# Performance work log

Measured on AMD Instinct MI355X. Metric: run time of the kernel, lower is better.

The kernel has to match this reference:

```python
import jax, jax.numpy as jnp
import numpy as np

B, N, C, H = 4, 1024, 1024, 16
DH = C // H  # 64
EPS = 1e-5   # nn.LayerNorm default


def _layernorm(x, g, b):
    m = x.mean(-1, keepdims=True)
    v = ((x - m) ** 2).mean(-1, keepdims=True)
    return (x - m) * jax.lax.rsqrt(v + EPS) * g + b


def _rot_half(x):
    d = x.shape[-1] // 2
    return jnp.concatenate([-x[..., d:], x[..., :d]], axis=-1)


def _apply_rope_cat(x, emb):
    # emb: [N, 2*DH] = sin || cos (torch tensor_split(2, -1) order)
    sin, cos = jnp.split(emb, 2, axis=-1)  # each [N, DH]
    return x * cos + _rot_half(x) * sin


def setup_inputs() -> dict:
    key = jax.random.key(0)
    ks = jax.random.split(key, 12)
    s = 0.02
    x = jax.random.normal(ks[0], (B, N, C), jnp.float32)
    delta_t_emb = jax.random.normal(ks[1], (B, N, C), jnp.float32)
    v_residual_v1 = jax.random.normal(ks[2], (B, H, N, DH), jnp.float32)
    # realistic rope table: sin||cos, each DH wide (freqs repeated twice for rotate_half)
    pos = jnp.arange(N, dtype=jnp.float32)
    inv_freq = 1.0 / (10000.0 ** (jnp.arange(0, DH // 2, dtype=jnp.float32) / (DH // 2)))
    freqs = pos[:, None] * inv_freq[None, :]          # [N, DH/2]
    freqs = jnp.concatenate([freqs, freqs], axis=-1)  # [N, DH]
    rope = jnp.concatenate([jnp.sin(freqs), jnp.cos(freqs)], axis=-1)  # [N, 2*DH]
    Wqkv = jax.random.normal(ks[3], (3 * C, C), jnp.float32) * s
    bqkv = jnp.zeros((3 * C,), jnp.float32)
    Wdt = jax.random.normal(ks[4], (3 * C, C), jnp.float32) * s
    bdt = jnp.zeros((3 * C,), jnp.float32)
    qn_g = jnp.ones((DH,), jnp.float32); qn_b = jnp.zeros((DH,), jnp.float32)
    kn_g = jnp.ones((DH,), jnp.float32); kn_b = jnp.zeros((DH,), jnp.float32)
    lamb1 = jnp.asarray(0.5, jnp.float32)
    lamb2 = jnp.asarray(0.5, jnp.float32)
    Wproj = jax.random.normal(ks[5], (C, C), jnp.float32) * s
    bproj = jnp.zeros((C,), jnp.float32)
    return {
        "x": x, "rope": rope, "delta_t_emb": delta_t_emb, "v_residual_v1": v_residual_v1,
        "Wqkv": Wqkv, "bqkv": bqkv, "Wdt": Wdt, "bdt": bdt,
        "qn_g": qn_g, "qn_b": qn_b, "kn_g": kn_g, "kn_b": kn_b,
        "lamb1": lamb1, "lamb2": lamb2, "Wproj": Wproj, "bproj": bproj,
    }


def reference(x, rope, delta_t_emb, v_residual_v1, Wqkv, bqkv, Wdt, bdt,
              qn_g, qn_b, kn_g, kn_b, lamb1, lamb2, Wproj, bproj):
    b, n, c = x.shape
    # fused QKV: [B,N,3C] -> [3,B,H,N,DH]
    qkv = (jnp.einsum('bnc,oc->bno', x, Wqkv) + bqkv).reshape(b, n, 3, H, DH)
    qkv = jnp.transpose(qkv, (2, 0, 3, 1, 4))
    q, k, v = qkv[0], qkv[1], qkv[2]
    # delta-t additive embeddings
    dqkv = (jnp.einsum('bnc,oc->bno', delta_t_emb, Wdt) + bdt).reshape(b, n, 3, H, DH)
    dqkv = jnp.transpose(dqkv, (2, 0, 3, 1, 4))
    q = q + dqkv[0]; k = k + dqkv[1]; v = v + dqkv[2]
    # value-residual mixing
    v = lamb1 * v + lamb2 * v_residual_v1
    # qk layernorm over head_dim
    q = _layernorm(q, qn_g, qn_b)
    k = _layernorm(k, kn_g, kn_b)
    # RoPE (num_prefix_tokens = 0, rotate_half=True)
    q = _apply_rope_cat(q, rope)
    k = _apply_rope_cat(k, rope)
    # SDPA, non-causal, no dropout
    scale = 1.0 / jnp.sqrt(jnp.asarray(DH, x.dtype))
    scores = jnp.einsum('bhqd,bhkd->bhqk', q, k) * scale
    attn = jax.nn.softmax(scores, axis=-1)
    out = jnp.einsum('bhqk,bhkd->bhqd', attn, v)
    # [B,H,N,DH] -> [B,N,C], output norm is Identity (scale_norm=False)
    out = jnp.transpose(out, (0, 2, 1, 3)).reshape(b, n, c)
    out = jnp.einsum('bnc,oc->bno', out, Wproj) + bproj
    return out
```

## Files before the change

### kernel.cpp

```cpp
#include <hip/hip_runtime.h>
#include <stdint.h>

typedef unsigned short u16;
typedef __attribute__((ext_vector_type(8))) short short8;
typedef __attribute__((ext_vector_type(4))) float f32x4;
typedef __attribute__((ext_vector_type(4))) unsigned short u16x4;

#define DEVI __device__ __forceinline__

DEVI u16 f2bf(float f) {
  uint32_t u = __builtin_bit_cast(uint32_t, f);
  u += 0x7fffu + ((u >> 16) & 1u);
  return (u16)(u >> 16);
}

DEVI void gload_lds16(const void* g, void* l) {
  __builtin_amdgcn_global_load_lds(
      (const __attribute__((address_space(1))) void*)g,
      (__attribute__((address_space(3))) void*)(uint32_t)(uintptr_t)l,
      16, 0, 0);
}

__global__ void cvt_cat_bf16(const float* __restrict__ a, const float* __restrict__ b,
                             u16* __restrict__ dst, long total) {
  for (long i = ((long)blockIdx.x * 256 + threadIdx.x) * 4; i < total;
       i += (long)gridDim.x * 1024) {
    const long row = i >> 11;
    const long c = i & 2047;
    const float* src = (c < 1024) ? (a + row * 1024 + c) : (b + row * 1024 + (c - 1024));
    const float4 v = *(const float4*)src;
    u16x4 o = {f2bf(v.x), f2bf(v.y), f2bf(v.z), f2bf(v.w)};
    *(u16x4*)(dst + i) = o;
  }
}

__global__ void cvt_bf16(const float* __restrict__ a, u16* __restrict__ dst, long total) {
  for (long i = ((long)blockIdx.x * 256 + threadIdx.x) * 4; i < total;
       i += (long)gridDim.x * 1024) {
    const float4 v = *(const float4*)(a + i);
    u16x4 o = {f2bf(v.x), f2bf(v.y), f2bf(v.z), f2bf(v.w)};
    *(u16x4*)(dst + i) = o;
  }
}

__global__ __launch_bounds__(256, 2)
void gemm_bt(const u16* __restrict__ A, const u16* __restrict__ B,
             float* __restrict__ C, const float* __restrict__ bias1,
             const float* __restrict__ bias2, int M, int N, int K) {
  __shared__ u16 As[128 * 32];
  __shared__ u16 Bs[128 * 32];
  const int t = threadIdx.x;
  const int w = t >> 6, l = t & 63;
  const int l15 = l & 15, lg = l >> 4;
  const int bm = blockIdx.x, bn = blockIdx.y;
  const int wr = (w >> 1) * 64, wc = (w & 1) * 64;
  f32x4 acc[4][4] = {};
  const int c0 = w * 64 + l;

  for (int kt = 0; kt < (K >> 5); ++kt) {
#pragma unroll
    for (int i = 0; i < 2; ++i) {
      const int c = i * 256 + c0;
      const int row = c >> 2, seg = c & 3;
      gload_lds16(A + (long)(bm * 128 + row) * K + kt * 32 + seg * 8,
                  (char*)As + w * 1024 + i * 4096);
      gload_lds16(B + (long)(bn * 128 + row) * K + kt * 32 + seg * 8,
                  (char*)Bs + w * 1024 + i * 4096);
    }
    __syncthreads();
    short8 af[4], bfr[4];
#pragma unroll
    for (int m = 0; m < 4; ++m)
      af[m] = *(const short8*)&As[(wr + m * 16 + l15) * 32 + lg * 8];
#pragma unroll
    for (int n = 0; n < 4; ++n)
      bfr[n] = *(const short8*)&Bs[(wc + n * 16 + l15) * 32 + lg * 8];
#pragma unroll
    for (int m = 0; m < 4; ++m)
#pragma unroll
      for (int n = 0; n < 4; ++n)
        acc[m][n] = __builtin_amdgcn_mfma_f32_16x16x32_bf16(af[m], bfr[n], acc[m][n], 0, 0, 0);
    __syncthreads();
  }
#pragma unroll
  for (int m = 0; m < 4; ++m) {
    const int row0 = bm * 128 + wr + m * 16 + lg * 4;
#pragma unroll
    for (int n = 0; n < 4; ++n) {
      const int col = bn * 128 + wc + n * 16 + l15;
      float bia = 0.f;
      if (bias1) bia += bias1[col];
      if (bias2) bia += bias2[col];
#pragma unroll
      for (int r = 0; r < 4; ++r)
        C[(long)(row0 + r) * N + col] = acc[m][n][r] + bia;
    }
  }
}

__global__ __launch_bounds__(256)
void fuse_qkv2(const float* __restrict__ qkv, const float* __restrict__ vres,
               const float* __restrict__ rope,
               const float* __restrict__ qg, const float* __restrict__ qb,
               const float* __restrict__ kg, const float* __restrict__ kb,
               const float* __restrict__ pl1, const float* __restrict__ pl2,
               u16* __restrict__ Q, u16* __restrict__ Ksw, u16* __restrict__ VTsw) {
  __shared__ u16 Vl[64][72];
  const int t = threadIdx.x, w = t >> 6, d = t & 63;
  const int bh = blockIdx.x, ntile = blockIdx.y;
  const int b = bh >> 4, h = bh & 15, n0 = ntile * 64;
  const float l1 = pl1[0], l2 = pl2[0];
  const float gq = qg[d], bq = qb[d];
  const float gk = kg[d], bk = kb[d];
  const float sgn = (d < 32) ? -1.f : 1.f;
  const int c = d >> 3, d7 = d & 7;

  for (int i = 0; i < 16; ++i) {
    const int nl = w * 16 + i;
    const int n = n0 + nl;
    const long base = ((long)(b * 1024 + n)) * 3072 + h * 64 + d;
    float q = qkv[base];
    float k = qkv[base + 1024];
    float v = qkv[base + 2048];
    v = l1 * v + l2 * vres[((long)(bh * 1024 + n)) * 64 + d];
    const float sinv = rope[n * 128 + d];
    const float cosv = rope[n * 128 + 64 + d];
    float s = q;
#pragma unroll
    for (int off = 1; off < 64; off <<= 1) s += __shfl_xor(s, off);
    const float qc = q - s * (1.f / 64.f);
    float vs = qc * qc;
#pragma unroll
    for (int off = 1; off < 64; off <<= 1) vs += __shfl_xor(vs, off);
    const float qn = qc * (1.f / sqrtf(vs * (1.f / 64.f) + 1e-5f)) * gq + bq;
    float s2 = k;
#pragma unroll
    for (int off = 1; off < 64; off <<= 1) s2 += __shfl_xor(s2, off);
    const float kc = k - s2 * (1.f / 64.f);
    float vs2 = kc * kc;
#pragma unroll
    for (int off = 1; off < 64; off <<= 1) vs2 += __shfl_xor(vs2, off);
    const float kn = kc * (1.f / sqrtf(vs2 * (1.f / 64.f) + 1e-5f)) * gk + bk;
    const float qo = __shfl_xor(qn, 32);
    const float ko = __shfl_xor(kn, 32);
    const float qr = qn * cosv + sgn * qo * sinv;
    const float kr = kn * cosv + sgn * ko * sinv;
    Q[(long)bh * 65536 + (long)n * 64 + d] = f2bf(qr);
    Ksw[(long)bh * 65536 + (long)n * 64 + ((c ^ (n & 7)) * 8 + d7)] = f2bf(kr);
    Vl[nl][d] = f2bf(v);
  }
  __syncthreads();
#pragma unroll
  for (int i = 0; i < 2; ++i) {
    const int task = i * 256 + t;
    const int dd = task >> 3, cc = task & 7;
    short8 o;
#pragma unroll
    for (int u = 0; u < 8; ++u) o[u] = (short)Vl[cc * 8 + u][dd];
    *(short8*)&VTsw[((long)(bh * 64 + dd)) * 1024 + n0 + ((cc ^ (dd & 7)) * 8)] = o;
  }
}

__global__ __launch_bounds__(256, 4)
void attn_fwd2(const u16* __restrict__ Q, const u16* __restrict__ Ksw,
               const u16* __restrict__ VTsw, u16* __restrict__ Out) {
  __shared__ u16 Kl[64 * 64];
  __shared__ u16 Vl[64 * 64];
  __shared__ u16 Pl[4][16 * 64];
  const int t = threadIdx.x, w = t >> 6, l = t & 63;
  const int l15 = l & 15, lg = l >> 4;
  const int x7 = l15 & 7;
  const int bh = blockIdx.x, q0 = blockIdx.y * 64;
  const long bo = (long)bh * 65536;
  u16* Plw = &Pl[w][0];

  const int qrow = q0 + w * 16 + l15;
  short8 qf[2];
#pragma unroll
  for (int ks = 0; ks < 2; ++ks)
    qf[ks] = *(const short8*)&Q[bo + (long)qrow * 64 + ks * 32 + lg * 8];

  f32x4 acc[4] = {};
  float m_run = -1e30f, l_run = 0.f;

  for (int kv = 0; kv < 16; ++kv) {
    const int kvb = kv * 64;
#pragma unroll
    for (int i = 0; i < 2; ++i) {
      const int idx = i * 256 + t;
      const int row = idx >> 3, seg = idx & 7;
      gload_lds16(Ksw + bo + (long)(kvb + row) * 64 + seg * 8, (char*)Kl + idx * 16);
      gload_lds16(VTsw + bo + (long)row * 1024 + kvb + seg * 8, (char*)Vl + idx * 16);
    }
    __syncthreads();
    f32x4 p[4];
#pragma unroll
    for (int mt = 0; mt < 4; ++mt) {
      f32x4 ps = {};
#pragma unroll
      for (int ks = 0; ks < 2; ++ks) {
        const short8 kf =
            *(const short8*)&Kl[(mt * 16 + l15) * 64 + (((ks * 4 + lg) ^ x7) * 8)];
        ps = __builtin_amdgcn_mfma_f32_16x16x32_bf16(kf, qf[ks], ps, 0, 0, 0);
      }
      p[mt] = ps;
    }
    float mx = p[0][0];
#pragma unroll
    for (int mt = 0; mt < 4; ++mt)
#pragma unroll
      for (int r = 0; r < 4; ++r) mx = fmaxf(mx, p[mt][r]);
    mx = fmaxf(mx, __shfl_xor(mx, 16));
    mx = fmaxf(mx, __shfl_xor(mx, 32));
    const float mnew = fmaxf(m_run, mx * 0.125f);
    const float alpha = __expf(m_run - mnew);
    m_run = mnew;
    float sum = 0.f;
#pragma unroll
    for (int mt = 0; mt < 4; ++mt)
#pragma unroll
      for (int r = 0; r < 4; ++r) {
        const float e = __expf(p[mt][r] * 0.125f - mnew);
        p[mt][r] = e;
        sum += e;
      }
    sum += __shfl_xor(sum, 16);
    sum += __shfl_xor(sum, 32);
    l_run = l_run * alpha + sum;
#pragma unroll
    for (int mt = 0; mt < 4; ++mt) {
      const int c = mt * 2 + (lg >> 1);
      char* bp = (char*)Plw + l15 * 128 + ((c ^ x7) * 16) + (lg & 1) * 8;
      *(uint32_t*)bp = (uint32_t)f2bf(p[mt][0]) | ((uint32_t)f2bf(p[mt][1]) << 16);
      *(uint32_t*)(bp + 4) = (uint32_t)f2bf(p[mt][2]) | ((uint32_t)f2bf(p[mt][3]) << 16);
    }
#pragma unroll
    for (int mt = 0; mt < 4; ++mt)
#pragma unroll
      for (int r = 0; r < 4; ++r) acc[mt][r] *= alpha;
#pragma unroll
    for (int ks = 0; ks < 2; ++ks) {
      const short8 pf =
          *(const short8*)((char*)Plw + l15 * 128 + (((ks * 4 + lg) ^ x7) * 16));
#pragma unroll
      for (int mt = 0; mt < 4; ++mt) {
        const short8 vf =
            *(const short8*)&Vl[(mt * 16 + l15) * 64 + (((ks * 4 + lg) ^ x7) * 8)];
        acc[mt] = __builtin_amdgcn_mfma_f32_16x16x32_bf16(vf, pf, acc[mt], 0, 0, 0);
      }
    }
    __syncthreads();
  }
  const int b = bh >> 4, h = bh & 15;
  const float inv = 1.f / l_run;
  const long obase = ((long)(b * 1024 + qrow)) * 1024 + h * 64;
#pragma unroll
  for (int mt = 0; mt < 4; ++mt) {
    const long o = obase + mt * 16 + lg * 4;
    *(uint32_t*)&Out[o] =
        (uint32_t)f2bf(acc[mt][0] * inv) | ((uint32_t)f2bf(acc[mt][1] * inv) << 16);
    *(uint32_t*)&Out[o + 2] =
        (uint32_t)f2bf(acc[mt][2] * inv) | ((uint32_t)f2bf(acc[mt][3] * inv) << 16);
  }
}

extern "C" void kernel_launch(void* const* d_in, const int* in_sizes, int n_in,
                              void* d_out, int out_size, void* d_ws, size_t ws_size,
                              hipStream_t stream) {
  const float* x     = (const float*)d_in[0];
  const float* rope  = (const float*)d_in[1];
  const float* dte   = (const float*)d_in[2];
  const float* vres  = (const float*)d_in[3];
  const float* Wqkv  = (const float*)d_in[4];
  const float* bqkv  = (const float*)d_in[5];
  const float* Wdt   = (const float*)d_in[6];
  const float* bdt   = (const float*)d_in[7];
  const float* qn_g  = (const float*)d_in[8];
  const float* qn_b  = (const float*)d_in[9];
  const float* kn_g  = (const float*)d_in[10];
  const float* kn_b  = (const float*)d_in[11];
  const float* l1    = (const float*)d_in[12];
  const float* l2    = (const float*)d_in[13];
  const float* Wproj = (const float*)d_in[14];
  const float* bproj = (const float*)d_in[15];
  float* out = (float*)d_out;

  char* ws = (char*)d_ws;
  u16*   A_cat = (u16*)(ws);
  u16*   W_cat = (u16*)(ws + 16777216);
  u16*   Wp    = (u16*)(ws + 29360128);
  float* qkv   = (float*)(ws + 31457280);
  u16*   Qb    = (u16*)(ws + 81788928);
  u16*   Ksw   = (u16*)(ws + 90177536);
  u16*   VTsw  = (u16*)(ws + 98566144);
  u16*   AO    = (u16*)(ws + 106954752);

  cvt_cat_bf16<<<2048, 256, 0, stream>>>(x, dte, A_cat, (long)4096 * 2048);
  cvt_cat_bf16<<<2048, 256, 0, stream>>>(Wqkv, Wdt, W_cat, (long)3072 * 2048);
  cvt_bf16<<<1024, 256, 0, stream>>>(Wproj, Wp, (long)1024 * 1024);
  gemm_bt<<<dim3(32, 24), 256, 0, stream>>>(A_cat, W_cat, qkv, bqkv, bdt, 4096, 3072, 2048);
  fuse_qkv2<<<dim3(64, 16), 256, 0, stream>>>(qkv, vres, rope, qn_g, qn_b, kn_g, kn_b,
                                              l1, l2, Qb, Ksw, VTsw);
  attn_fwd2<<<dim3(64, 16), 256, 0, stream>>>(Qb, Ksw, VTsw, AO);
  gemm_bt<<<dim3(32, 8), 256, 0, stream>>>(AO, Wp, out, bproj, nullptr, 4096, 1024, 1024);
}
```

Baseline: 173.2 us.

## Add 256x256-tile pipelined GEMM with swizzled LDS for fused QKV projection

Adds a new gemm256 kernel that computes 256x256 output tiles with 512 threads and a 4-deep LDS ring buffer filled by direct global-to-LDS loads issued three K-tiles ahead, with explicit vmcnt waits. It also XOR-swizzles the LDS layout to avoid bank conflicts and remaps block IDs to group tiles for L2 locality. The QKV GEMM launch now uses this kernel instead of the 128x128 gemm_bt. The aim is more reuse per loaded byte and overlap of memory with MFMA work. In exchange it uses 128KB of LDS per block and only 192 blocks, so occupancy is low and the grid may not fill all CUs evenly.

```diff
diff --git a/kernel.cpp b/kernel.cpp
--- a/kernel.cpp
+++ b/kernel.cpp
@@ -88,6 +88,92 @@
 #pragma unroll
     for (int n = 0; n < 4; ++n) {
       const int col = bn * 128 + wc + n * 16 + l15;
+      float bia = 0.f;
+      if (bias1) bia += bias1[col];
+      if (bias2) bia += bias2[col];
+#pragma unroll
+      for (int r = 0; r < 4; ++r)
+        C[(long)(row0 + r) * N + col] = acc[m][n][r] + bia;
+    }
+  }
+}
+
+__global__ __launch_bounds__(512, 2)
+void gemm256(const u16* __restrict__ A, const u16* __restrict__ B,
+             float* __restrict__ C, const float* __restrict__ bias1,
+             const float* __restrict__ bias2, int M, int N, int K) {
+  __shared__ u16 lds[4][16384];
+  const int t = threadIdx.x;
+  const int w = t >> 6, l = t & 63;
+  const int l15 = l & 15, lg = l >> 4;
+  const int wr = w >> 2, wc = w & 3;
+  const int nbn = N >> 8;
+  const int nb = gridDim.x;
+  const int bid = blockIdx.x;
+  const int lid = ((nb & 7) == 0) ? ((bid & 7) * (nb >> 3) + (bid >> 3)) : bid;
+  const int bm = lid / nbn, bn = lid % nbn;
+  const long rowA0 = (long)bm * 256;
+  const long rowB0 = (long)bn * 256;
+  const int nkt = K >> 5;
+
+  const int su = (l & 7) ^ (l >> 3);
+  const int rsub = 2 * (l >> 3) + (su >> 2);
+  const int sg = su & 3;
+  const int sfr = (lg + 4 * (l15 & 1)) ^ (l15 >> 1);
+
+  f32x4 acc[8][4] = {};
+
+#define STAGE(KT)                                                              \
+  {                                                                            \
+    const int _b = (KT) & 3;                                                   \
+    _Pragma("unroll") for (int i = 0; i < 2; ++i) {                            \
+      const int r = i * 128 + w * 16 + rsub;                                   \
+      gload_lds16(A + (rowA0 + r) * K + (KT) * 32 + sg * 8,                    \
+                  (char*)&lds[_b][(i * 64 + w * 8) * 64]);                     \
+      gload_lds16(B + (rowB0 + r) * K + (KT) * 32 + sg * 8,                    \
+                  (char*)&lds[_b][8192 + (i * 64 + w * 8) * 64]);              \
+    }                                                                          \
+  }
+
+#define TILE(KT, VMSTR, DO_STAGE)                                              \
+  {                                                                            \
+    asm volatile("s_waitcnt vmcnt(" VMSTR ")" ::: "memory");                   \
+    __builtin_amdgcn_s_barrier();                                              \
+    asm volatile("" ::: "memory");                                             \
+    __builtin_amdgcn_sched_barrier(0);                                         \
+    if (DO_STAGE) STAGE((KT) + 3);                                             \
+    const u16* bufp = lds[(KT) & 3];                                           \
+    short8 bfr[4];                                                             \
+    _Pragma("unroll") for (int n = 0; n < 4; ++n) {                            \
+      const int p = wc * 32 + n * 8 + (l15 >> 1);                              \
+      bfr[n] = *(const short8*)&bufp[8192 + p * 64 + sfr * 8];                 \
+    }                                                                          \
+    __builtin_amdgcn_s_setprio(1);                                             \
+    _Pragma("unroll") for (int m = 0; m < 8; ++m) {                            \
+      const int p = wr * 64 + m * 8 + (l15 >> 1);                              \
+      const short8 af = *(const short8*)&bufp[p * 64 + sfr * 8];               \
+      _Pragma("unroll") for (int n = 0; n < 4; ++n)                            \
+        acc[m][n] = __builtin_amdgcn_mfma_f32_16x16x32_bf16(af, bfr[n],        \
+                                                            acc[m][n], 0, 0, 0); \
+    }                                                                          \
+    __builtin_amdgcn_s_setprio(0);                                             \
+  }
+
+  STAGE(0)
+  STAGE(1)
+  STAGE(2)
+  for (int kt = 0; kt < nkt - 2; ++kt) TILE(kt, "8", (kt + 3 < nkt))
+  TILE(nkt - 2, "4", false)
+  TILE(nkt - 1, "0", false)
+#undef TILE
+#undef STAGE
+
+#pragma unroll
+  for (int m = 0; m < 8; ++m) {
+    const int row0 = bm * 256 + wr * 128 + m * 16 + lg * 4;
+#pragma unroll
+    for (int n = 0; n < 4; ++n) {
+      const int col = bn * 256 + wc * 64 + n * 16 + l15;
       float bia = 0.f;
       if (bias1) bia += bias1[col];
       if (bias2) bia += bias2[col];
@@ -298,7 +384,7 @@
   cvt_cat_bf16<<<2048, 256, 0, stream>>>(x, dte, A_cat, (long)4096 * 2048);
   cvt_cat_bf16<<<2048, 256, 0, stream>>>(Wqkv, Wdt, W_cat, (long)3072 * 2048);
   cvt_bf16<<<1024, 256, 0, stream>>>(Wproj, Wp, (long)1024 * 1024);
-  gemm_bt<<<dim3(32, 24), 256, 0, stream>>>(A_cat, W_cat, qkv, bqkv, bdt, 4096, 3072, 2048);
+  gemm256<<<192, 512, 0, stream>>>(A_cat, W_cat, qkv, bqkv, bdt, 4096, 3072, 2048);
   fuse_qkv2<<<dim3(64, 16), 256, 0, stream>>>(qkv, vres, rope, qn_g, qn_b, kn_g, kn_b,
                                               l1, l2, Qb, Ksw, VTsw);
   attn_fwd2<<<dim3(64, 16), 256, 0, stream>>>(Qb, Ksw, VTsw, AO);
```

Result: no change. 173.6 us (+0.3%).

## Replace QKV GEMM with 256x256 pipelined kernel writing bf16 output

Applied to the files above, without the earlier changes.

Adds a new 512-thread GEMM that uses 256x256 tiles, a 4-stage LDS ring with swizzled global-to-LDS loads, split MFMA phases and XCD-aware block remapping. It is used for the fused QKV+delta-t projection, and its output is stored as bf16 instead of fp32, which halves the intermediate traffic read by fuse_qkv2. The aim is higher MFMA utilisation and less memory traffic. The cost is extra rounding of the pre-layernorm q/k/v values and only 192 blocks for the large tile size.

```diff
diff --git a/kernel.cpp b/kernel.cpp
--- a/kernel.cpp
+++ b/kernel.cpp
@@ -12,6 +12,11 @@
   uint32_t u = __builtin_bit_cast(uint32_t, f);
   u += 0x7fffu + ((u >> 16) & 1u);
   return (u16)(u >> 16);
+}
+
+DEVI float bf2f(u16 u) {
+  uint32_t v = ((uint32_t)u) << 16;
+  return __builtin_bit_cast(float, v);
 }
 
 DEVI void gload_lds16(const void* g, void* l) {
@@ -98,8 +103,147 @@
   }
 }
 
+__global__ __launch_bounds__(512, 2)
+void gemm256(const u16* __restrict__ A, const u16* __restrict__ B,
+             u16* __restrict__ Cb, const float* __restrict__ bias1,
+             const float* __restrict__ bias2, int M, int N, int K) {
+  __shared__ u16 lds[4][16384];
+  const int t = threadIdx.x;
+  const int w = t >> 6, l = t & 63;
+  const int l15 = l & 15, lg = l >> 4;
+  const int wr = w >> 2, wc = w & 3;
+  const int nbn = N >> 8;
+  const int nb = gridDim.x;
+  const int bid = blockIdx.x;
+  const int lid = ((nb & 7) == 0) ? ((bid & 7) * (nb >> 3) + (bid >> 3)) : bid;
+  const int bm = lid / nbn, bn = lid % nbn;
+  const long rowA0 = (long)bm * 256;
+  const long rowB0 = (long)bn * 256;
+  const int nkt = K >> 5;
+
+  const int su = (l & 7) ^ (l >> 3);
+  const int rsub = 2 * (l >> 3) + (su >> 2);
+  const int sg = su & 3;
+  const int sfr = (lg + 4 * (l15 & 1)) ^ (l15 >> 1);
+
+  f32x4 acc[8][4] = {};
+  short8 alo[4], ahi[4], b0[4], b1[4];
+
+#define STAGE_A(KT)                                                           \
+  {                                                                           \
+    const int _b = (KT) & 3;                                                  \
+    _Pragma("unroll") for (int i = 0; i < 2; ++i) {                           \
+      const int r = i * 128 + w * 16 + rsub;                                  \
+      gload_lds16(A + (rowA0 + r) * K + (KT) * 32 + sg * 8,                   \
+                  (char*)&lds[_b][(i * 64 + w * 8) * 64]);                    \
+    }                                                                         \
+  }
+#define STAGE_B(KT)                                                           \
+  {                                                                           \
+    const int _b = (KT) & 3;                                                  \
+    _Pragma("unroll") for (int i = 0; i < 2; ++i) {                           \
+      const int r = i * 128 + w * 16 + rsub;                                  \
+      gload_lds16(B + (rowB0 + r) * K + (KT) * 32 + sg * 8,                   \
+                  (char*)&lds[_b][8192 + (i * 64 + w * 8) * 64]);             \
+    }                                                                         \
+  }
+
+#define TILE(KT, BC, BN_, VM, LG1, DO_STAGE, DO_NEXT)                         \
+  {                                                                           \
+    const u16* bufp = lds[(KT) & 3];                                          \
+           \
+    _Pragma("unroll") for (int m = 0; m < 4; ++m) {                           \
+      const int p = wr * 64 + (m + 4) * 8 + (l15 >> 1);                       \
+      ahi[m] = *(const short8*)&bufp[p * 64 + sfr * 8];                       \
+    }                                                                         \
+    if (DO_STAGE) STAGE_A((KT) + 3);                                          \
+    asm volatile("s_waitcnt vmcnt(" VM ")" ::: "memory");                     \
+    __builtin_amdgcn_sched_barrier(0);                                        \
+    __builtin_amdgcn_s_barrier();                                             \
+    asm volatile("s_waitcnt lgkmcnt(4)" ::: "memory");                        \
+    __builtin_amdgcn_sched_barrier(0);                                        \
+    __builtin_amdgcn_s_setprio(1);                                            \
+    _Pragma("unroll") for (int m = 0; m < 4; ++m)                             \
+      _Pragma("unroll") for (int n = 0; n < 4; ++n)                           \
+        acc[m][n] = __builtin_amdgcn_mfma_f32_16x16x32_bf16(alo[m], BC[n],    \
+                                                            acc[m][n], 0, 0, 0); \
+    __builtin_amdgcn_s_setprio(0);                                            \
+    __builtin_amdgcn_sched_barrier(0);                                        \
+    __builtin_amdgcn_s_barrier();                                             \
+                    \
+    if (DO_NEXT) {                                                            \
+      const u16* bnp = lds[((KT) + 1) & 3];                                   \
+      _Pragma("unroll") for (int m = 0; m < 4; ++m) {                         \
+        const int p = wr * 64 + m * 8 + (l15 >> 1);                           \
+        alo[m] = *(const short8*)&bnp[p * 64 + sfr * 8];                      \
+      }                                                                       \
+      _Pragma("unroll") for (int n = 0; n < 4; ++n) {                         \
+        const int p = wc * 32 + n * 8 + (l15 >> 1);                           \
+        BN_[n] = *(const short8*)&bnp[8192 + p * 64 + sfr * 8];               \
+      }                                                                       \
+    }                                                                         \
+    if (DO_STAGE) STAGE_B((KT) + 3);                                          \
+    __builtin_amdgcn_sched_barrier(0);                                        \
+    __builtin_amdgcn_s_barrier();                                             \
+    asm volatile("s_waitcnt lgkmcnt(" LG1 ")" ::: "memory");                  \
+    __builtin_amdgcn_sched_barrier(0);                                        \
+    __builtin_amdgcn_s_setprio(1);                                            \
+    _Pragma("unroll") for (int m = 0; m < 4; ++m)                             \
+      _Pragma("unroll") for (int n = 0; n < 4; ++n)                           \
+        acc[m + 4][n] = __builtin_amdgcn_mfma_f32_16x16x32_bf16(              \
+            ahi[m], BC[n], acc[m + 4][n], 0, 0, 0);                           \
+    __builtin_amdgcn_s_setprio(0);                                            \
+    __builtin_amdgcn_sched_barrier(0);                                        \
+    __builtin_amdgcn_s_barrier();                                             \
+  }
+
+  STAGE_A(0); STAGE_B(0);
+  STAGE_A(1); STAGE_B(1);
+  STAGE_A(2); STAGE_B(2);
+  asm volatile("s_waitcnt vmcnt(8)" ::: "memory");
+  __builtin_amdgcn_sched_barrier(0);
+  __builtin_amdgcn_s_barrier();
+#pragma unroll
+  for (int m = 0; m < 4; ++m) {
+    const int p = wr * 64 + m * 8 + (l15 >> 1);
+    alo[m] = *(const short8*)&lds[0][p * 64 + sfr * 8];
+  }
+#pragma unroll
+  for (int n = 0; n < 4; ++n) {
+    const int p = wc * 32 + n * 8 + (l15 >> 1);
+    b0[n] = *(const short8*)&lds[0][8192 + p * 64 + sfr * 8];
+  }
+
+  for (int kt = 0; kt < nkt - 4; kt += 2) {
+    TILE(kt, b0, b1, "6", "8", 1, 1)
+    TILE(kt + 1, b1, b0, "6", "8", 1, 1)
+  }
+  TILE(nkt - 4, b0, b1, "6", "8", 1, 1)
+  TILE(nkt - 3, b1, b0, "4", "8", 0, 1)
+  TILE(nkt - 2, b0, b1, "0", "8", 0, 1)
+  TILE(nkt - 1, b1, b0, "0", "0", 0, 0)
+#undef TILE
+#undef STAGE_A
+#undef STAGE_B
+
+#pragma unroll
+  for (int m = 0; m < 8; ++m) {
+    const int row0 = bm * 256 + wr * 128 + m * 16 + lg * 4;
+#pragma unroll
+    for (int n = 0; n < 4; ++n) {
+      const int col = bn * 256 + wc * 64 + n * 16 + l15;
+      float bia = 0.f;
+      if (bias1) bia += bias1[col];
+      if (bias2) bia += bias2[col];
+#pragma unroll
+      for (int r = 0; r < 4; ++r)
+        Cb[(long)(row0 + r) * N + col] = f2bf(acc[m][n][r] + bia);
+    }
+  }
+}
+
 __global__ __launch_bounds__(256)
-void fuse_qkv2(const float* __restrict__ qkv, const float* __restrict__ vres,
+void fuse_qkv2(const u16* __restrict__ qkv, const float* __restrict__ vres,
                const float* __restrict__ rope,
                const float* __restrict__ qg, const float* __restrict__ qb,
                const float* __restrict__ kg, const float* __restrict__ kb,
@@ -119,9 +263,9 @@
     const int nl = w * 16 + i;
     const int n = n0 + nl;
     const long base = ((long)(b * 1024 + n)) * 3072 + h * 64 + d;
-    float q = qkv[base];
-    float k = qkv[base + 1024];
-    float v = qkv[base + 2048];
+    float q = bf2f(qkv[base]);
+    float k = bf2f(qkv[base + 1024]);
+    float v = bf2f(qkv[base + 2048]);
     v = l1 * v + l2 * vres[((long)(bh * 1024 + n)) * 64 + d];
     const float sinv = rope[n * 128 + d];
     const float cosv = rope[n * 128 + 64 + d];
@@ -289,17 +433,17 @@
   u16*   A_cat = (u16*)(ws);
   u16*   W_cat = (u16*)(ws + 16777216);
   u16*   Wp    = (u16*)(ws + 29360128);
-  float* qkv   = (float*)(ws + 31457280);
-  u16*   Qb    = (u16*)(ws + 81788928);
-  u16*   Ksw   = (u16*)(ws + 90177536);
-  u16*   VTsw  = (u16*)(ws + 98566144);
-  u16*   AO    = (u16*)(ws + 106954752);
+  u16*   qkvb  = (u16*)(ws + 31457280);
+  u16*   Qb    = (u16*)(ws + 56623104);
+  u16*   Ksw   = (u16*)(ws + 65011712);
+  u16*   VTsw  = (u16*)(ws + 73400320);
+  u16*   AO    = (u16*)(ws + 81788928);
 
   cvt_cat_bf16<<<2048, 256, 0, stream>>>(x, dte, A_cat, (long)4096 * 2048);
   cvt_cat_bf16<<<2048, 256, 0, stream>>>(Wqkv, Wdt, W_cat, (long)3072 * 2048);
   cvt_bf16<<<1024, 256, 0, stream>>>(Wproj, Wp, (long)1024 * 1024);
-  gemm_bt<<<dim3(32, 24), 256, 0, stream>>>(A_cat, W_cat, qkv, bqkv, bdt, 4096, 3072, 2048);
-  fuse_qkv2<<<dim3(64, 16), 256, 0, stream>>>(qkv, vres, rope, qn_g, qn_b, kn_g, kn_b,
+  gemm256<<<192, 512, 0, stream>>>(A_cat, W_cat, qkvb, bqkv, bdt, 4096, 3072, 2048);
+  fuse_qkv2<<<dim3(64, 16), 256, 0, stream>>>(qkvb, vres, rope, qn_g, qn_b, kn_g, kn_b,
                                               l1, l2, Qb, Ksw, VTsw);
   attn_fwd2<<<dim3(64, 16), 256, 0, stream>>>(Qb, Ksw, VTsw, AO);
   gemm_bt<<<dim3(32, 8), 256, 0, stream>>>(AO, Wp, out, bproj, nullptr, 4096, 1024, 1024);
```

Measured after the change: 171.1 us. No clear change (-1.2%).

## Store QKV GEMM output in bf16 and double-buffer attention with 128-row query tiles

Applied to the files above, without the earlier changes.

The QKV projection GEMM now writes bf16 instead of fp32, which halves the intermediate write and the read in fuse_qkv2, at the cost of an extra rounding before layernorm. The attention kernel is rewritten to process two 64-row query sub-tiles per block so each K/V tile load is shared by both. It also double-buffers the K/V LDS tiles so the next tile's global-to-LDS copy overlaps the current tile's compute. The grid shrinks to 512 blocks and occupancy hints drop to 2 blocks per CU, which may hurt latency hiding.

```diff
diff --git a/kernel.cpp b/kernel.cpp
--- a/kernel.cpp
+++ b/kernel.cpp
@@ -12,6 +12,11 @@
   uint32_t u = __builtin_bit_cast(uint32_t, f);
   u += 0x7fffu + ((u >> 16) & 1u);
   return (u16)(u >> 16);
+}
+
+DEVI float bf2f(u16 u) {
+  uint32_t v = ((uint32_t)u) << 16;
+  return __builtin_bit_cast(float, v);
 }
 
 DEVI void gload_lds16(const void* g, void* l) {
@@ -98,8 +103,63 @@
   }
 }
 
+__global__ __launch_bounds__(256, 2)
+void gemm_bt_b16(const u16* __restrict__ A, const u16* __restrict__ B,
+                 u16* __restrict__ C, const float* __restrict__ bias1,
+                 const float* __restrict__ bias2, int M, int N, int K) {
+  __shared__ u16 As[128 * 32];
+  __shared__ u16 Bs[128 * 32];
+  const int t = threadIdx.x;
+  const int w = t >> 6, l = t & 63;
+  const int l15 = l & 15, lg = l >> 4;
+  const int bm = blockIdx.x, bn = blockIdx.y;
+  const int wr = (w >> 1) * 64, wc = (w & 1) * 64;
+  f32x4 acc[4][4] = {};
+  const int c0 = w * 64 + l;
+
+  for (int kt = 0; kt < (K >> 5); ++kt) {
+#pragma unroll
+    for (int i = 0; i < 2; ++i) {
+      const int c = i * 256 + c0;
+      const int row = c >> 2, seg = c & 3;
+      gload_lds16(A + (long)(bm * 128 + row) * K + kt * 32 + seg * 8,
+                  (char*)As + w * 1024 + i * 4096);
+      gload_lds16(B + (long)(bn * 128 + row) * K + kt * 32 + seg * 8,
+                  (char*)Bs + w * 1024 + i * 4096);
+    }
+    __syncthreads();
+    short8 af[4], bfr[4];
+#pragma unroll
+    for (int m = 0; m < 4; ++m)
+      af[m] = *(const short8*)&As[(wr + m * 16 + l15) * 32 + lg * 8];
+#pragma unroll
+    for (int n = 0; n < 4; ++n)
+      bfr[n] = *(const short8*)&Bs[(wc + n * 16 + l15) * 32 + lg * 8];
+#pragma unroll
+    for (int m = 0; m < 4; ++m)
+#pragma unroll
+      for (int n = 0; n < 4; ++n)
+        acc[m][n] = __builtin_amdgcn_mfma_f32_16x16x32_bf16(af[m], bfr[n], acc[m][n], 0, 0, 0);
+    __syncthreads();
+  }
+#pragma unroll
+  for (int m = 0; m < 4; ++m) {
+    const int row0 = bm * 128 + wr + m * 16 + lg * 4;
+#pragma unroll
+    for (int n = 0; n < 4; ++n) {
+      const int col = bn * 128 + wc + n * 16 + l15;
+      float bia = 0.f;
+      if (bias1) bia += bias1[col];
+      if (bias2) bia += bias2[col];
+#pragma unroll
+      for (int r = 0; r < 4; ++r)
+        C[(long)(row0 + r) * N + col] = f2bf(acc[m][n][r] + bia);
+    }
+  }
+}
+
 __global__ __launch_bounds__(256)
-void fuse_qkv2(const float* __restrict__ qkv, const float* __restrict__ vres,
+void fuse_qkv2(const u16* __restrict__ qkv, const float* __restrict__ vres,
                const float* __restrict__ rope,
                const float* __restrict__ qg, const float* __restrict__ qb,
                const float* __restrict__ kg, const float* __restrict__ kb,
@@ -119,9 +179,9 @@
     const int nl = w * 16 + i;
     const int n = n0 + nl;
     const long base = ((long)(b * 1024 + n)) * 3072 + h * 64 + d;
-    float q = qkv[base];
-    float k = qkv[base + 1024];
-    float v = qkv[base + 2048];
+    float q = bf2f(qkv[base]);
+    float k = bf2f(qkv[base + 1024]);
+    float v = bf2f(qkv[base + 2048]);
     v = l1 * v + l2 * vres[((long)(bh * 1024 + n)) * 64 + d];
     const float sinv = rope[n * 128 + d];
     const float cosv = rope[n * 128 + 64 + d];
@@ -161,38 +221,31 @@
   }
 }
 
-__global__ __launch_bounds__(256, 4)
-void attn_fwd2(const u16* __restrict__ Q, const u16* __restrict__ Ksw,
+__global__ __launch_bounds__(256, 2)
+void attn_fwd3(const u16* __restrict__ Q, const u16* __restrict__ Ksw,
                const u16* __restrict__ VTsw, u16* __restrict__ Out) {
-  __shared__ u16 Kl[64 * 64];
-  __shared__ u16 Vl[64 * 64];
-  __shared__ u16 Pl[4][16 * 64];
+  __shared__ u16 Kl[2][64 * 64];
+  __shared__ u16 Vl[2][64 * 64];
+  __shared__ u16 Pl[4][2][16 * 64];
   const int t = threadIdx.x, w = t >> 6, l = t & 63;
   const int l15 = l & 15, lg = l >> 4;
   const int x7 = l15 & 7;
-  const int bh = blockIdx.x, q0 = blockIdx.y * 64;
+  const int bh = blockIdx.x, q0 = blockIdx.y * 128;
   const long bo = (long)bh * 65536;
-  u16* Plw = &Pl[w][0];
-
-  const int qrow = q0 + w * 16 + l15;
-  short8 qf[2];
-#pragma unroll
-  for (int ks = 0; ks < 2; ++ks)
-    qf[ks] = *(const short8*)&Q[bo + (long)qrow * 64 + ks * 32 + lg * 8];
-
-  f32x4 acc[4] = {};
-  float m_run = -1e30f, l_run = 0.f;
-
-  for (int kv = 0; kv < 16; ++kv) {
-    const int kvb = kv * 64;
-#pragma unroll
-    for (int i = 0; i < 2; ++i) {
-      const int idx = i * 256 + t;
-      const int row = idx >> 3, seg = idx & 7;
-      gload_lds16(Ksw + bo + (long)(kvb + row) * 64 + seg * 8, (char*)Kl + idx * 16);
-      gload_lds16(VTsw + bo + (long)row * 1024 + kvb + seg * 8, (char*)Vl + idx * 16);
-    }
-    __syncthreads();
+
+  short8 qf[2][2];
+#pragma unroll
+  for (int sub = 0; sub < 2; ++sub)
+#pragma unroll
+    for (int ks = 0; ks < 2; ++ks)
+      qf[sub][ks] = *(const short8*)&Q[bo + (long)(q0 + sub * 64 + w * 16 + l15) * 64 +
+                                       ks * 32 + lg * 8];
+
+  f32x4 acc[2][4] = {};
+  float m_run[2] = {-1e30f, -1e30f};
+  float l_run[2] = {0.f, 0.f};
+
+  auto subt = [&](int kv, int cur, int sub) {
     f32x4 p[4];
 #pragma unroll
     for (int mt = 0; mt < 4; ++mt) {
@@ -200,8 +253,8 @@
 #pragma unroll
       for (int ks = 0; ks < 2; ++ks) {
         const short8 kf =
-            *(const short8*)&Kl[(mt * 16 + l15) * 64 + (((ks * 4 + lg) ^ x7) * 8)];
-        ps = __builtin_amdgcn_mfma_f32_16x16x32_bf16(kf, qf[ks], ps, 0, 0, 0);
+            *(const short8*)&Kl[cur][(mt * 16 + l15) * 64 + (((ks * 4 + lg) ^ x7) * 8)];
+        ps = __builtin_amdgcn_mfma_f32_16x16x32_bf16(kf, qf[sub][ks], ps, 0, 0, 0);
       }
       p[mt] = ps;
     }
@@ -212,9 +265,9 @@
       for (int r = 0; r < 4; ++r) mx = fmaxf(mx, p[mt][r]);
     mx = fmaxf(mx, __shfl_xor(mx, 16));
     mx = fmaxf(mx, __shfl_xor(mx, 32));
-    const float mnew = fmaxf(m_run, mx * 0.125f);
-    const float alpha = __expf(m_run - mnew);
-    m_run = mnew;
+    const float mnew = fmaxf(m_run[sub], mx * 0.125f);
+    const float alpha = __expf(m_run[sub] - mnew);
+    m_run[sub] = mnew;
     float sum = 0.f;
 #pragma unroll
     for (int mt = 0; mt < 4; ++mt)
@@ -226,41 +279,81 @@
       }
     sum += __shfl_xor(sum, 16);
     sum += __shfl_xor(sum, 32);
-    l_run = l_run * alpha + sum;
+    l_run[sub] = l_run[sub] * alpha + sum;
+    char* Plw = (char*)&Pl[w][sub][0];
 #pragma unroll
     for (int mt = 0; mt < 4; ++mt) {
       const int c = mt * 2 + (lg >> 1);
-      char* bp = (char*)Plw + l15 * 128 + ((c ^ x7) * 16) + (lg & 1) * 8;
+      char* bp = Plw + l15 * 128 + ((c ^ x7) * 16) + (lg & 1) * 8;
       *(uint32_t*)bp = (uint32_t)f2bf(p[mt][0]) | ((uint32_t)f2bf(p[mt][1]) << 16);
       *(uint32_t*)(bp + 4) = (uint32_t)f2bf(p[mt][2]) | ((uint32_t)f2bf(p[mt][3]) << 16);
     }
 #pragma unroll
     for (int mt = 0; mt < 4; ++mt)
 #pragma unroll
-      for (int r = 0; r < 4; ++r) acc[mt][r] *= alpha;
+      for (int r = 0; r < 4; ++r) acc[sub][mt][r] *= alpha;
 #pragma unroll
     for (int ks = 0; ks < 2; ++ks) {
-      const short8 pf =
-          *(const short8*)((char*)Plw + l15 * 128 + (((ks * 4 + lg) ^ x7) * 16));
+      const short8 pf = *(const short8*)(Plw + l15 * 128 + (((ks * 4 + lg) ^ x7) * 16));
 #pragma unroll
       for (int mt = 0; mt < 4; ++mt) {
         const short8 vf =
-            *(const short8*)&Vl[(mt * 16 + l15) * 64 + (((ks * 4 + lg) ^ x7) * 8)];
-        acc[mt] = __builtin_amdgcn_mfma_f32_16x16x32_bf16(vf, pf, acc[mt], 0, 0, 0);
+            *(const short8*)&Vl[cur][(mt * 16 + l15) * 64 + (((ks * 4 + lg) ^ x7) * 8)];
+        acc[sub][mt] = __builtin_amdgcn_mfma_f32_16x16x32_bf16(vf, pf, acc[sub][mt], 0, 0, 0);
       }
     }
-    __syncthreads();
-  }
+  };
+
+#define ASTAGE(KV, BUF)                                                          \
+  {                                                                              \
+    _Pragma("unroll") for (int i = 0; i < 2; ++i) {                              \
+      const int idx = i * 256 + t;                                               \
+      const int row = idx >> 3, seg = idx & 7;                                   \
+      gload_lds16(Ksw + bo + (long)((KV) * 64 + row) * 64 + seg * 8,             \
+                  (char*)&Kl[BUF][0] + idx * 16);                                \
+      gload_lds16(VTsw + bo + (long)row * 1024 + (KV) * 64 + seg * 8,            \
+                  (char*)&Vl[BUF][0] + idx * 16);                                \
+    }                                                                            \
+  }
+
+#define AITER(KV, CUR, DO_STAGE)                                                 \
+  {                                                                              \
+    if (DO_STAGE) ASTAGE((KV) + 1, (CUR) ^ 1);                                   \
+    subt((KV), (CUR), 0);                                                        \
+    subt((KV), (CUR), 1);                                                        \
+    asm volatile("s_waitcnt vmcnt(0)" ::: "memory");                             \
+    __builtin_amdgcn_sched_barrier(0);                                           \
+    __builtin_amdgcn_s_barrier();                                                \
+    __builtin_amdgcn_sched_barrier(0);                                           \
+  }
+
+  ASTAGE(0, 0)
+  asm volatile("s_waitcnt vmcnt(0)" ::: "memory");
+  __builtin_amdgcn_sched_barrier(0);
+  __builtin_amdgcn_s_barrier();
+  __builtin_amdgcn_sched_barrier(0);
+
+  for (int kp = 0; kp < 8; ++kp) {
+    AITER(2 * kp, 0, 1)
+    AITER(2 * kp + 1, 1, (kp < 7))
+  }
+#undef AITER
+#undef ASTAGE
+
   const int b = bh >> 4, h = bh & 15;
-  const float inv = 1.f / l_run;
-  const long obase = ((long)(b * 1024 + qrow)) * 1024 + h * 64;
-#pragma unroll
-  for (int mt = 0; mt < 4; ++mt) {
-    const long o = obase + mt * 16 + lg * 4;
-    *(uint32_t*)&Out[o] =
-        (uint32_t)f2bf(acc[mt][0] * inv) | ((uint32_t)f2bf(acc[mt][1] * inv) << 16);
-    *(uint32_t*)&Out[o + 2] =
-        (uint32_t)f2bf(acc[mt][2] * inv) | ((uint32_t)f2bf(acc[mt][3] * inv) << 16);
+#pragma unroll
+  for (int sub = 0; sub < 2; ++sub) {
+    const int qrow = q0 + sub * 64 + w * 16 + l15;
+    const float inv = 1.f / l_run[sub];
+    const long obase = ((long)(b * 1024 + qrow)) * 1024 + h * 64;
+#pragma unroll
+    for (int mt = 0; mt < 4; ++mt) {
+      const long o = obase + mt * 16 + lg * 4;
+      *(uint32_t*)&Out[o] = (uint32_t)f2bf(acc[sub][mt][0] * inv) |
+                            ((uint32_t)f2bf(acc[sub][mt][1] * inv) << 16);
+      *(uint32_t*)&Out[o + 2] = (uint32_t)f2bf(acc[sub][mt][2] * inv) |
+                                ((uint32_t)f2bf(acc[sub][mt][3] * inv) << 16);
+    }
   }
 }
 
@@ -289,18 +382,19 @@
   u16*   A_cat = (u16*)(ws);
   u16*   W_cat = (u16*)(ws + 16777216);
   u16*   Wp    = (u16*)(ws + 29360128);
-  float* qkv   = (float*)(ws + 31457280);
-  u16*   Qb    = (u16*)(ws + 81788928);
-  u16*   Ksw   = (u16*)(ws + 90177536);
-  u16*   VTsw  = (u16*)(ws + 98566144);
-  u16*   AO    = (u16*)(ws + 106954752);
+  u16*   qkvb  = (u16*)(ws + 31457280);
+  u16*   Qb    = (u16*)(ws + 56623104);
+  u16*   Ksw   = (u16*)(ws + 65011712);
+  u16*   VTsw  = (u16*)(ws + 73400320);
+  u16*   AO    = (u16*)(ws + 81788928);
 
   cvt_cat_bf16<<<2048, 256, 0, stream>>>(x, dte, A_cat, (long)4096 * 2048);
   cvt_cat_bf16<<<2048, 256, 0, stream>>>(Wqkv, Wdt, W_cat, (long)3072 * 2048);
   cvt_bf16<<<1024, 256, 0, stream>>>(Wproj, Wp, (long)1024 * 1024);
-  gemm_bt<<<dim3(32, 24), 256, 0, stream>>>(A_cat, W_cat, qkv, bqkv, bdt, 4096, 3072, 2048);
-  fuse_qkv2<<<dim3(64, 16), 256, 0, stream>>>(qkv, vres, rope, qn_g, qn_b, kn_g, kn_b,
+  gemm_bt_b16<<<dim3(32, 24), 256, 0, stream>>>(A_cat, W_cat, qkvb, bqkv, bdt,
+                                                4096, 3072, 2048);
+  fuse_qkv2<<<dim3(64, 16), 256, 0, stream>>>(qkvb, vres, rope, qn_g, qn_b, kn_g, kn_b,
                                               l1, l2, Qb, Ksw, VTsw);
-  attn_fwd2<<<dim3(64, 16), 256, 0, stream>>>(Qb, Ksw, VTsw, AO);
+  attn_fwd3<<<dim3(64, 8), 256, 0, stream>>>(Qb, Ksw, VTsw, AO);
   gemm_bt<<<dim3(32, 8), 256, 0, stream>>>(AO, Wp, out, bproj, nullptr, 4096, 1024, 1024);
 }
```

Result: no change. 170.8 us (-1.4%).
